# Kernel tuning notes

Measured on AMD Instinct MI355X. Metric: run time of the kernel, lower is better.

The kernel has to match this reference:

```python
import jax, jax.numpy as jnp
import numpy as np

KH = KW = 3
STRIDE = 1
PAD = 1
DIL = 1


def _bilinear_sample(x, py, px):
    """Zero-padded bilinear sampling.
    x: [B, C, H, W]; py, px: [B, K2, Ho, Wo] float sample coords.
    returns [B, C, K2, Ho, Wo].
    """
    B, C, H, W = x.shape
    y0 = jnp.floor(py)
    x0 = jnp.floor(px)
    wy1 = py - y0
    wx1 = px - x0
    wy0 = 1.0 - wy1
    wx0 = 1.0 - wx1
    xf = x.reshape(B, C, H * W)

    def gather(iy, ix):
        valid = (iy >= 0) & (iy <= H - 1) & (ix >= 0) & (ix <= W - 1)
        iyc = jnp.clip(iy, 0, H - 1).astype(jnp.int32)
        ixc = jnp.clip(ix, 0, W - 1).astype(jnp.int32)
        idx = (iyc * W + ixc).reshape(B, 1, -1)  # [B,1,K2*Ho*Wo]
        v = jnp.take_along_axis(xf, idx, axis=2)
        v = v.reshape(B, C, *iy.shape[1:])
        return v * valid[:, None].astype(x.dtype)

    return (gather(y0, x0) * (wy0 * wx0)[:, None]
            + gather(y0, x0 + 1) * (wy0 * wx1)[:, None]
            + gather(y0 + 1, x0) * (wy1 * wx0)[:, None]
            + gather(y0 + 1, x0 + 1) * (wy1 * wx1)[:, None])


def setup_inputs() -> dict:
    key = jax.random.key(0)
    k1, k2, k3, k4 = jax.random.split(key, 4)
    B, C, H, W = 8, 64, 128, 128
    Cout = 64
    K2 = KH * KW
    x = jax.random.normal(k1, (B, C, H, W), dtype=jnp.float32)
    offset = jax.random.normal(k2, (B, 2 * K2, H, W), dtype=jnp.float32)
    mask = jax.random.uniform(k3, (B, K2, H, W), dtype=jnp.float32)
    n = C * KH * KW
    stdv = 1.0 / np.sqrt(n)
    weight = jax.random.uniform(k4, (Cout, C, KH, KW), dtype=jnp.float32,
                                minval=-stdv, maxval=stdv)
    bias = jnp.zeros((Cout,), dtype=jnp.float32)
    return {"x": x, "offset": offset, "mask": mask, "weight": weight, "bias": bias}


def reference(x, offset, mask, weight, bias):
    B, C, H, W = x.shape
    Cout, Cin, kh, kw = weight.shape
    K2 = kh * kw
    Ho = (H + 2 * PAD - (DIL * (kh - 1) + 1)) // STRIDE + 1
    Wo = (W + 2 * PAD - (DIL * (kw - 1) + 1)) // STRIDE + 1
    # offset channels come interleaved per kernel location: ::2 -> x, 1::2 -> y
    off = offset.reshape(B, K2, 2, Ho, Wo)
    dx = off[:, :, 0]  # [B,K2,Ho,Wo]
    dy = off[:, :, 1]
    base_y = (STRIDE * jnp.arange(Ho) - PAD).astype(x.dtype)  # [Ho]
    base_x = (STRIDE * jnp.arange(Wo) - PAD).astype(x.dtype)  # [Wo]
    ky = (DIL * jnp.arange(kh)).astype(x.dtype)
    kx = (DIL * jnp.arange(kw)).astype(x.dtype)
    koff_y = jnp.repeat(ky, kw)  # [K2]
    koff_x = jnp.tile(kx, kh)    # [K2]
    py = base_y[None, None, :, None] + koff_y[None, :, None, None] + dy
    px = base_x[None, None, None, :] + koff_x[None, :, None, None] + dx
    sampled = _bilinear_sample(x, py, px)          # [B,C,K2,Ho,Wo]
    sampled = sampled * mask[:, None]              # modulation
    w = weight.reshape(Cout, Cin * K2)
    cols = sampled.reshape(B, Cin * K2, Ho, Wo)
    out = jnp.einsum('bqhw,oq->bohw', cols, w) + bias[None, :, None, None]
    return out
```

## Files before the change

kernel.cpp:

```cpp
#include <hip/hip_runtime.h>
#include <hip/hip_bf16.h>


constexpr int B    = 8;
constexpr int C    = 64;
constexpr int H    = 128;
constexpr int W    = 128;
constexpr int COUT = 64;
constexpr int K2   = 9;
constexpr int HW   = H * W;

typedef __attribute__((ext_vector_type(8))) short bf16x8;
typedef __attribute__((ext_vector_type(4))) float f32x4;

constexpr int LDSS = 72;

__global__ __launch_bounds__(256) void transpose_x_kernel(
    const float* __restrict__ x, short* __restrict__ xt) {
    __shared__ float tbuf[64][65];
    const int blk  = blockIdx.x;
    const int b    = blk >> 8;
    const int hwb  = (blk & 255) * 64;
    const int lane = threadIdx.x & 63;
    const int grp  = threadIdx.x >> 6;
    const float* xb = x + (size_t)b * C * HW;
#pragma unroll
    for (int r = 0; r < 16; ++r) {
        const int c = grp * 16 + r;
        tbuf[c][lane] = xb[c * HW + hwb + lane];
    }
    __syncthreads();
    short* xo = xt + (size_t)b * HW * C;
#pragma unroll
    for (int r = 0; r < 16; ++r) {
        const int hw_l = grp * 16 + r;
        union { __hip_bfloat16 h; short s; } u;
        u.h = __float2bfloat16(tbuf[lane][hw_l]);
        xo[(size_t)(hwb + hw_l) * C + lane] = u.s;
    }
}

__global__ __launch_bounds__(256) void pack_w_kernel(
    const float* __restrict__ w, short* __restrict__ wfrag) {
    int id = blockIdx.x * blockDim.x + threadIdx.x;
    if (id >= COUT * C * K2) return;
    const int j    = id & 7;
    const int lane = (id >> 3) & 63;
    const int mt   = (id >> 9) & 3;
    const int kk   = (id >> 11) & 1;
    const int k    = id >> 12;
    const int m    = mt * 16 + (lane & 15);
    const int q    = lane >> 4;
    const int c    = kk * 32 + q * 8 + j;
    union { __hip_bfloat16 h; short s; } u;
    u.h = __float2bfloat16(w[(m * C + c) * K2 + k]);
    wfrag[id] = u.s;
}

__global__ __launch_bounds__(256, 6) void mdcn_mfma_kernel(
    const short* __restrict__ xt,
    const float* __restrict__ offset,
    const float* __restrict__ mask,
    const short* __restrict__ wfrag,
    const float* __restrict__ bias,
    float* __restrict__ out) {

    __shared__ short smem[64 * LDSS];
    __shared__ float offs[2 * K2 * 64];
    __shared__ float msks[K2 * 64];

    const int wg   = blockIdx.x;
    const int b    = wg & 7;
    const int t    = wg >> 3;
    const int ho   = t >> 1;
    const int px0  = (t & 1) * 64;

    const int tid  = threadIdx.x;
    const int wave = tid >> 6;
    const int lane = tid & 63;
    const int col  = lane & 15;
    const int q    = lane >> 4;
    const int spx  = tid >> 2;
    const int cq   = (tid & 3) * 16;

    for (int f = tid; f < 2 * K2 * 64; f += 256) {
        const int ch = f >> 6, i = f & 63;
        offs[f] = offset[(((size_t)b * 2 * K2 + ch) * H + ho) * W + px0 + i];
    }
    for (int f = tid; f < K2 * 64; f += 256) {
        const int ch = f >> 6, i = f & 63;
        msks[f] = mask[(((size_t)b * K2 + ch) * H + ho) * W + px0 + i];
    }

    const short* xb = xt + (size_t)b * HW * C;
    f32x4 acc[4];
#pragma unroll
    for (int mt = 0; mt < 4; ++mt) acc[mt] = (f32x4)0.0f;

    __syncthreads();

    for (int k = 0; k < K2; ++k) {
        const int ky = k / 3, kx = k % 3;
        const float dx = offs[(2 * k    ) * 64 + spx];
        const float dy = offs[(2 * k + 1) * 64 + spx];
        const float mm = msks[k * 64 + spx];
        const int wo = px0 + spx;

        const float py = (float)(ho - 1 + ky) + dy;
        const float px = (float)(wo - 1 + kx) + dx;
        const float y0f = floorf(py), x0f = floorf(px);
        const float wy1 = py - y0f,   wx1 = px - x0f;
        const float wy0 = 1.0f - wy1, wx0 = 1.0f - wx1;
        const int iy0 = (int)y0f, ix0 = (int)x0f;
        const int iy1 = iy0 + 1,  ix1 = ix0 + 1;
        const bool vy0 = (iy0 >= 0) & (iy0 < H);
        const bool vy1 = (iy1 >= 0) & (iy1 < H);
        const bool vx0 = (ix0 >= 0) & (ix0 < W);
        const bool vx1 = (ix1 >= 0) & (ix1 < W);
        const float w00 = (vy0 & vx0) ? wy0 * wx0 * mm : 0.0f;
        const float w01 = (vy0 & vx1) ? wy0 * wx1 * mm : 0.0f;
        const float w10 = (vy1 & vx0) ? wy1 * wx0 * mm : 0.0f;
        const float w11 = (vy1 & vx1) ? wy1 * wx1 * mm : 0.0f;
        const int cy0 = min(max(iy0, 0), H - 1);
        const int cy1 = min(max(iy1, 0), H - 1);
        const int cx0 = min(max(ix0, 0), W - 1);
        const int cx1 = min(max(ix1, 0), W - 1);

        const short* s00 = xb + (cy0 * W + cx0) * C + cq;
        const short* s01 = xb + (cy0 * W + cx1) * C + cq;
        const short* s10 = xb + (cy1 * W + cx0) * C + cq;
        const short* s11 = xb + (cy1 * W + cx1) * C + cq;

        bf16x8 g00[2], g01[2], g10[2], g11[2];
#pragma unroll
        for (int j = 0; j < 2; ++j) {
            g00[j] = *(const bf16x8*)(s00 + j * 8);
            g01[j] = *(const bf16x8*)(s01 + j * 8);
            g10[j] = *(const bf16x8*)(s10 + j * 8);
            g11[j] = *(const bf16x8*)(s11 + j * 8);
        }

        short* sdst = smem + spx * LDSS + cq;
#pragma unroll
        for (int j = 0; j < 2; ++j) {
            union U8 { bf16x8 s; __hip_bfloat162 h2[4]; };
            U8 u00{g00[j]}, u01{g01[j]}, u10{g10[j]}, u11{g11[j]}, r;
#pragma unroll
            for (int p = 0; p < 4; ++p) {
                const float2 f00 = __bfloat1622float2(u00.h2[p]);
                const float2 f01 = __bfloat1622float2(u01.h2[p]);
                const float2 f10 = __bfloat1622float2(u10.h2[p]);
                const float2 f11 = __bfloat1622float2(u11.h2[p]);
                float2 v;
                v.x = w00 * f00.x + w01 * f01.x + w10 * f10.x + w11 * f11.x;
                v.y = w00 * f00.y + w01 * f01.y + w10 * f10.y + w11 * f11.y;
                r.h2[p] = __float22bfloat162_rn(v);
            }
            *(bf16x8*)(sdst + j * 8) = r.s;
        }
        __syncthreads();

        const bf16x8* wf = (const bf16x8*)wfrag;
#pragma unroll
        for (int kk = 0; kk < 2; ++kk) {
            const bf16x8 bfrag =
                *(const bf16x8*)(smem + (wave * 16 + col) * LDSS + kk * 32 + q * 8);
#pragma unroll
            for (int mt = 0; mt < 4; ++mt) {
                const bf16x8 afrag = wf[((k * 2 + kk) * 4 + mt) * 64 + lane];
                acc[mt] = __builtin_amdgcn_mfma_f32_16x16x32_bf16(
                    afrag, bfrag, acc[mt], 0, 0, 0);
            }
        }
        __syncthreads();
    }

    const int wo = px0 + wave * 16 + col;
#pragma unroll
    for (int mt = 0; mt < 4; ++mt) {
#pragma unroll
        for (int r = 0; r < 4; ++r) {
            const int o = mt * 16 + q * 4 + r;
            out[(((size_t)b * COUT + o) * H + ho) * W + wo] = acc[mt][r] + bias[o];
        }
    }
}

__global__ __launch_bounds__(256) void mdcn_direct_kernel(
    const float* __restrict__ x, const float* __restrict__ offset,
    const float* __restrict__ mask, const float* __restrict__ wsrc,
    const float* __restrict__ bias, float* __restrict__ out) {
    const int p  = blockIdx.x * blockDim.x + threadIdx.x;
    const int wo = p & (W - 1);
    const int ho = (p >> 7) & (H - 1);
    const int b  = p >> 14;
    float acc[COUT];
#pragma unroll
    for (int o = 0; o < COUT; ++o) acc[o] = bias[o];
    const float* xb = x + b * C * HW;
    for (int k = 0; k < K2; ++k) {
        const int ky = k / 3, kx = k % 3;
        const float dx = offset[((b * 2 * K2 + 2 * k    ) * H + ho) * W + wo];
        const float dy = offset[((b * 2 * K2 + 2 * k + 1) * H + ho) * W + wo];
        const float m  = mask  [((b * K2     + k        ) * H + ho) * W + wo];
        const float py = (float)(ho - 1 + ky) + dy;
        const float px = (float)(wo - 1 + kx) + dx;
        const float y0f = floorf(py), x0f = floorf(px);
        const float wy1 = py - y0f, wx1 = px - x0f;
        const float wy0 = 1.0f - wy1, wx0 = 1.0f - wx1;
        const int iy0 = (int)y0f, ix0 = (int)x0f;
        const int iy1 = iy0 + 1, ix1 = ix0 + 1;
        const bool vy0 = (iy0 >= 0) & (iy0 < H);
        const bool vy1 = (iy1 >= 0) & (iy1 < H);
        const bool vx0 = (ix0 >= 0) & (ix0 < W);
        const bool vx1 = (ix1 >= 0) & (ix1 < W);
        const float w00 = (vy0 & vx0) ? wy0 * wx0 * m : 0.0f;
        const float w01 = (vy0 & vx1) ? wy0 * wx1 * m : 0.0f;
        const float w10 = (vy1 & vx0) ? wy1 * wx0 * m : 0.0f;
        const float w11 = (vy1 & vx1) ? wy1 * wx1 * m : 0.0f;
        const int cy0 = min(max(iy0, 0), H - 1);
        const int cy1 = min(max(iy1, 0), H - 1);
        const int cx0 = min(max(ix0, 0), W - 1);
        const int cx1 = min(max(ix1, 0), W - 1);
        const int o00 = cy0 * W + cx0, o01 = cy0 * W + cx1;
        const int o10 = cy1 * W + cx0, o11 = cy1 * W + cx1;
        for (int c = 0; c < C; ++c) {
            const float* xp = xb + c * HW;
            const float val = w00 * xp[o00] + w01 * xp[o01] +
                              w10 * xp[o10] + w11 * xp[o11];
#pragma unroll
            for (int o = 0; o < COUT; ++o)
                acc[o] += wsrc[(o * C + c) * K2 + k] * val;
        }
    }
    float* op = out + ((size_t)b * COUT) * HW + ho * W + wo;
#pragma unroll
    for (int o = 0; o < COUT; ++o) op[o * HW] = acc[o];
}

extern "C" void kernel_launch(void* const* d_in, const int* in_sizes, int n_in,
                              void* d_out, int out_size, void* d_ws, size_t ws_size,
                              hipStream_t stream) {
    const float* x      = (const float*)d_in[0];
    const float* offset = (const float*)d_in[1];
    const float* mask   = (const float*)d_in[2];
    const float* weight = (const float*)d_in[3];
    const float* bias   = (const float*)d_in[4];
    float* out          = (float*)d_out;

    const size_t xt_bytes = (size_t)B * HW * C * sizeof(short);
    const size_t wf_bytes = (size_t)COUT * C * K2 * sizeof(short);
    if (ws_size >= xt_bytes + wf_bytes) {
        short* xt    = (short*)d_ws;
        short* wfrag = (short*)((char*)d_ws + xt_bytes);
        transpose_x_kernel<<<B * (HW / 64), 256, 0, stream>>>(x, xt);
        pack_w_kernel<<<(COUT * C * K2 + 255) / 256, 256, 0, stream>>>(weight, wfrag);
        mdcn_mfma_kernel<<<2 * B * H, 256, 0, stream>>>(xt, offset, mask, wfrag, bias, out);
    } else {
        mdcn_direct_kernel<<<(B * HW) / 256, 256, 0, stream>>>(
            x, offset, mask, weight, bias, out);
    }
}
```

Measured before the change: 152.7 us.

## Build MFMA B-fragments directly in registers, dropping LDS staging and barriers

Each lane now computes the bilinear samples for exactly the pixel/channel slice its MFMA B-fragment needs, so the LDS tile and both per-tap __syncthreads are removed. Offsets and mask are loaded straight from global memory into per-lane register arrays instead of being staged in shared memory. Launch bounds occupancy hint drops from 6 to 4 to allow more registers. The cost is redundant offset/weight computation across the 4 q-lanes sharing a pixel and higher register pressure.

```diff
diff --git a/kernel.cpp b/kernel.cpp
--- a/kernel.cpp
+++ b/kernel.cpp
@@ -12,8 +12,6 @@
 
 typedef __attribute__((ext_vector_type(8))) short bf16x8;
 typedef __attribute__((ext_vector_type(4))) float f32x4;
-
-constexpr int LDSS = 72;
 
 __global__ __launch_bounds__(256) void transpose_x_kernel(
     const float* __restrict__ x, short* __restrict__ xt) {
@@ -57,7 +55,7 @@
     wfrag[id] = u.s;
 }
 
-__global__ __launch_bounds__(256, 6) void mdcn_mfma_kernel(
+__global__ __launch_bounds__(256, 4) void mdcn_mfma_kernel(
     const short* __restrict__ xt,
     const float* __restrict__ offset,
     const float* __restrict__ mask,
@@ -65,10 +63,6 @@
     const float* __restrict__ bias,
     float* __restrict__ out) {
 
-    __shared__ short smem[64 * LDSS];
-    __shared__ float offs[2 * K2 * 64];
-    __shared__ float msks[K2 * 64];
-
     const int wg   = blockIdx.x;
     const int b    = wg & 7;
     const int t    = wg >> 3;
@@ -80,34 +74,28 @@
     const int lane = tid & 63;
     const int col  = lane & 15;
     const int q    = lane >> 4;
-    const int spx  = tid >> 2;
-    const int cq   = (tid & 3) * 16;
-
-    for (int f = tid; f < 2 * K2 * 64; f += 256) {
-        const int ch = f >> 6, i = f & 63;
-        offs[f] = offset[(((size_t)b * 2 * K2 + ch) * H + ho) * W + px0 + i];
-    }
-    for (int f = tid; f < K2 * 64; f += 256) {
-        const int ch = f >> 6, i = f & 63;
-        msks[f] = mask[(((size_t)b * K2 + ch) * H + ho) * W + px0 + i];
-    }
-
-    const short* xb = xt + (size_t)b * HW * C;
+    const int wo   = px0 + wave * 16 + col;
+
+    float dxs[K2], dys[K2], ms[K2];
+#pragma unroll
+    for (int k = 0; k < K2; ++k) {
+        dxs[k] = offset[(((size_t)b * 2 * K2 + 2 * k    ) * H + ho) * W + wo];
+        dys[k] = offset[(((size_t)b * 2 * K2 + 2 * k + 1) * H + ho) * W + wo];
+        ms[k]  = mask  [(((size_t)b * K2     + k        ) * H + ho) * W + wo];
+    }
+
+    const short*  xb = xt + (size_t)b * HW * C;
+    const bf16x8* wf = (const bf16x8*)wfrag;
+
     f32x4 acc[4];
 #pragma unroll
     for (int mt = 0; mt < 4; ++mt) acc[mt] = (f32x4)0.0f;
-
-    __syncthreads();
 
     for (int k = 0; k < K2; ++k) {
         const int ky = k / 3, kx = k % 3;
-        const float dx = offs[(2 * k    ) * 64 + spx];
-        const float dy = offs[(2 * k + 1) * 64 + spx];
-        const float mm = msks[k * 64 + spx];
-        const int wo = px0 + spx;
-
-        const float py = (float)(ho - 1 + ky) + dy;
-        const float px = (float)(wo - 1 + kx) + dx;
+        const float mm = ms[k];
+        const float py = (float)(ho - 1 + ky) + dys[k];
+        const float px = (float)(wo - 1 + kx) + dxs[k];
         const float y0f = floorf(py), x0f = floorf(px);
         const float wy1 = py - y0f,   wx1 = px - x0f;
         const float wy0 = 1.0f - wy1, wx0 = 1.0f - wx1;
@@ -125,26 +113,21 @@
         const int cy1 = min(max(iy1, 0), H - 1);
         const int cx0 = min(max(ix0, 0), W - 1);
         const int cx1 = min(max(ix1, 0), W - 1);
-
-        const short* s00 = xb + (cy0 * W + cx0) * C + cq;
-        const short* s01 = xb + (cy0 * W + cx1) * C + cq;
-        const short* s10 = xb + (cy1 * W + cx0) * C + cq;
-        const short* s11 = xb + (cy1 * W + cx1) * C + cq;
-
-        bf16x8 g00[2], g01[2], g10[2], g11[2];
-#pragma unroll
-        for (int j = 0; j < 2; ++j) {
-            g00[j] = *(const bf16x8*)(s00 + j * 8);
-            g01[j] = *(const bf16x8*)(s01 + j * 8);
-            g10[j] = *(const bf16x8*)(s10 + j * 8);
-            g11[j] = *(const bf16x8*)(s11 + j * 8);
-        }
-
-        short* sdst = smem + spx * LDSS + cq;
-#pragma unroll
-        for (int j = 0; j < 2; ++j) {
+        const int b00 = (cy0 * W + cx0) * C;
+        const int b01 = (cy0 * W + cx1) * C;
+        const int b10 = (cy1 * W + cx0) * C;
+        const int b11 = (cy1 * W + cx1) * C;
+
+        bf16x8 bfrag[2];
+#pragma unroll
+        for (int kk = 0; kk < 2; ++kk) {
+            const int co = kk * 32 + q * 8;
+            const bf16x8 g00 = *(const bf16x8*)(xb + b00 + co);
+            const bf16x8 g01 = *(const bf16x8*)(xb + b01 + co);
+            const bf16x8 g10 = *(const bf16x8*)(xb + b10 + co);
+            const bf16x8 g11 = *(const bf16x8*)(xb + b11 + co);
             union U8 { bf16x8 s; __hip_bfloat162 h2[4]; };
-            U8 u00{g00[j]}, u01{g01[j]}, u10{g10[j]}, u11{g11[j]}, r;
+            U8 u00{g00}, u01{g01}, u10{g10}, u11{g11}, rr;
 #pragma unroll
             for (int p = 0; p < 4; ++p) {
                 const float2 f00 = __bfloat1622float2(u00.h2[p]);
@@ -154,28 +137,20 @@
                 float2 v;
                 v.x = w00 * f00.x + w01 * f01.x + w10 * f10.x + w11 * f11.x;
                 v.y = w00 * f00.y + w01 * f01.y + w10 * f10.y + w11 * f11.y;
-                r.h2[p] = __float22bfloat162_rn(v);
+                rr.h2[p] = __float22bfloat162_rn(v);
             }
-            *(bf16x8*)(sdst + j * 8) = r.s;
+            bfrag[kk] = rr.s;
         }
-        __syncthreads();
-
-        const bf16x8* wf = (const bf16x8*)wfrag;
-#pragma unroll
-        for (int kk = 0; kk < 2; ++kk) {
-            const bf16x8 bfrag =
-                *(const bf16x8*)(smem + (wave * 16 + col) * LDSS + kk * 32 + q * 8);
-#pragma unroll
-            for (int mt = 0; mt < 4; ++mt) {
-                const bf16x8 afrag = wf[((k * 2 + kk) * 4 + mt) * 64 + lane];
+
+#pragma unroll
+        for (int kk = 0; kk < 2; ++kk)
+#pragma unroll
+            for (int mt = 0; mt < 4; ++mt)
                 acc[mt] = __builtin_amdgcn_mfma_f32_16x16x32_bf16(
-                    afrag, bfrag, acc[mt], 0, 0, 0);
-            }
-        }
-        __syncthreads();
-    }
-
-    const int wo = px0 + wave * 16 + col;
+                    wf[((k * 2 + kk) * 4 + mt) * 64 + lane], bfrag[kk],
+                    acc[mt], 0, 0, 0);
+    }
+
 #pragma unroll
     for (int mt = 0; mt < 4; ++mt) {
 #pragma unroll
```

Measured after the change: 184.1 us. 20.6% more time.

## Warp-specialize deformable conv into gather producers and MFMA consumers with double buffering

Applied to the files above, without the earlier changes.

The block grows to 512 threads. Four waves do the bilinear gather and write the interpolated bf16 columns into a double-buffered LDS tile. The other four waves load weight fragments and run the MFMA accumulation on the previous tile. The aim is to overlap the latency-heavy gather with the matrix multiply, where before each wave did both with two barriers per kernel tap. The cost is that only half the resident waves now issue gather loads, so memory-latency hiding for the gather may drop, and LDS use doubles.

```diff
diff --git a/kernel.cpp b/kernel.cpp
--- a/kernel.cpp
+++ b/kernel.cpp
@@ -57,7 +57,7 @@
     wfrag[id] = u.s;
 }
 
-__global__ __launch_bounds__(256, 6) void mdcn_mfma_kernel(
+__global__ __launch_bounds__(512, 4) void mdcn_pc_kernel(
     const short* __restrict__ xt,
     const float* __restrict__ offset,
     const float* __restrict__ mask,
@@ -65,7 +65,7 @@
     const float* __restrict__ bias,
     float* __restrict__ out) {
 
-    __shared__ short smem[64 * LDSS];
+    __shared__ short smem[2][64 * LDSS];
     __shared__ float offs[2 * K2 * 64];
     __shared__ float msks[K2 * 64];
 
@@ -77,111 +77,113 @@
 
     const int tid  = threadIdx.x;
     const int wave = tid >> 6;
-    const int lane = tid & 63;
-    const int col  = lane & 15;
-    const int q    = lane >> 4;
-    const int spx  = tid >> 2;
-    const int cq   = (tid & 3) * 16;
-
-    for (int f = tid; f < 2 * K2 * 64; f += 256) {
+
+    for (int f = tid; f < 2 * K2 * 64; f += 512) {
         const int ch = f >> 6, i = f & 63;
         offs[f] = offset[(((size_t)b * 2 * K2 + ch) * H + ho) * W + px0 + i];
     }
-    for (int f = tid; f < K2 * 64; f += 256) {
+    for (int f = tid; f < K2 * 64; f += 512) {
         const int ch = f >> 6, i = f & 63;
         msks[f] = mask[(((size_t)b * K2 + ch) * H + ho) * W + px0 + i];
     }
-
-    const short* xb = xt + (size_t)b * HW * C;
-    f32x4 acc[4];
-#pragma unroll
-    for (int mt = 0; mt < 4; ++mt) acc[mt] = (f32x4)0.0f;
-
     __syncthreads();
 
-    for (int k = 0; k < K2; ++k) {
-        const int ky = k / 3, kx = k % 3;
-        const float dx = offs[(2 * k    ) * 64 + spx];
-        const float dy = offs[(2 * k + 1) * 64 + spx];
-        const float mm = msks[k * 64 + spx];
-        const int wo = px0 + spx;
-
-        const float py = (float)(ho - 1 + ky) + dy;
-        const float px = (float)(wo - 1 + kx) + dx;
-        const float y0f = floorf(py), x0f = floorf(px);
-        const float wy1 = py - y0f,   wx1 = px - x0f;
-        const float wy0 = 1.0f - wy1, wx0 = 1.0f - wx1;
-        const int iy0 = (int)y0f, ix0 = (int)x0f;
-        const int iy1 = iy0 + 1,  ix1 = ix0 + 1;
-        const bool vy0 = (iy0 >= 0) & (iy0 < H);
-        const bool vy1 = (iy1 >= 0) & (iy1 < H);
-        const bool vx0 = (ix0 >= 0) & (ix0 < W);
-        const bool vx1 = (ix1 >= 0) & (ix1 < W);
-        const float w00 = (vy0 & vx0) ? wy0 * wx0 * mm : 0.0f;
-        const float w01 = (vy0 & vx1) ? wy0 * wx1 * mm : 0.0f;
-        const float w10 = (vy1 & vx0) ? wy1 * wx0 * mm : 0.0f;
-        const float w11 = (vy1 & vx1) ? wy1 * wx1 * mm : 0.0f;
-        const int cy0 = min(max(iy0, 0), H - 1);
-        const int cy1 = min(max(iy1, 0), H - 1);
-        const int cx0 = min(max(ix0, 0), W - 1);
-        const int cx1 = min(max(ix1, 0), W - 1);
-
-        const short* s00 = xb + (cy0 * W + cx0) * C + cq;
-        const short* s01 = xb + (cy0 * W + cx1) * C + cq;
-        const short* s10 = xb + (cy1 * W + cx0) * C + cq;
-        const short* s11 = xb + (cy1 * W + cx1) * C + cq;
-
-        bf16x8 g00[2], g01[2], g10[2], g11[2];
-#pragma unroll
-        for (int j = 0; j < 2; ++j) {
-            g00[j] = *(const bf16x8*)(s00 + j * 8);
-            g01[j] = *(const bf16x8*)(s01 + j * 8);
-            g10[j] = *(const bf16x8*)(s10 + j * 8);
-            g11[j] = *(const bf16x8*)(s11 + j * 8);
-        }
-
-        short* sdst = smem + spx * LDSS + cq;
-#pragma unroll
-        for (int j = 0; j < 2; ++j) {
-            union U8 { bf16x8 s; __hip_bfloat162 h2[4]; };
-            U8 u00{g00[j]}, u01{g01[j]}, u10{g10[j]}, u11{g11[j]}, r;
-#pragma unroll
-            for (int p = 0; p < 4; ++p) {
-                const float2 f00 = __bfloat1622float2(u00.h2[p]);
-                const float2 f01 = __bfloat1622float2(u01.h2[p]);
-                const float2 f10 = __bfloat1622float2(u10.h2[p]);
-                const float2 f11 = __bfloat1622float2(u11.h2[p]);
-                float2 v;
-                v.x = w00 * f00.x + w01 * f01.x + w10 * f10.x + w11 * f11.x;
-                v.y = w00 * f00.y + w01 * f01.y + w10 * f10.y + w11 * f11.y;
-                r.h2[p] = __float22bfloat162_rn(v);
+    if (wave < 4) {
+        const int spx = tid >> 2;
+        const int cq  = (tid & 3) * 16;
+        const int wo  = px0 + spx;
+        const short* xb = xt + (size_t)b * HW * C;
+
+        for (int k = 0; k < K2; ++k) {
+            const int ky = k / 3, kx = k % 3;
+            const float dx = offs[(2 * k    ) * 64 + spx];
+            const float dy = offs[(2 * k + 1) * 64 + spx];
+            const float mm = msks[k * 64 + spx];
+            const float py = (float)(ho - 1 + ky) + dy;
+            const float px = (float)(wo - 1 + kx) + dx;
+            const float y0f = floorf(py), x0f = floorf(px);
+            const float wy1 = py - y0f,   wx1 = px - x0f;
+            const float wy0 = 1.0f - wy1, wx0 = 1.0f - wx1;
+            const int iy0 = (int)y0f, ix0 = (int)x0f;
+            const int iy1 = iy0 + 1,  ix1 = ix0 + 1;
+            const bool vy0 = (iy0 >= 0) & (iy0 < H);
+            const bool vy1 = (iy1 >= 0) & (iy1 < H);
+            const bool vx0 = (ix0 >= 0) & (ix0 < W);
+            const bool vx1 = (ix1 >= 0) & (ix1 < W);
+            const float w00 = (vy0 & vx0) ? wy0 * wx0 * mm : 0.0f;
+            const float w01 = (vy0 & vx1) ? wy0 * wx1 * mm : 0.0f;
+            const float w10 = (vy1 & vx0) ? wy1 * wx0 * mm : 0.0f;
+            const float w11 = (vy1 & vx1) ? wy1 * wx1 * mm : 0.0f;
+            const int cy0 = min(max(iy0, 0), H - 1);
+            const int cy1 = min(max(iy1, 0), H - 1);
+            const int cx0 = min(max(ix0, 0), W - 1);
+            const int cx1 = min(max(ix1, 0), W - 1);
+            const short* s00 = xb + (cy0 * W + cx0) * C + cq;
+            const short* s01 = xb + (cy0 * W + cx1) * C + cq;
+            const short* s10 = xb + (cy1 * W + cx0) * C + cq;
+            const short* s11 = xb + (cy1 * W + cx1) * C + cq;
+
+            short* dst = &smem[k & 1][spx * LDSS + cq];
+#pragma unroll
+            for (int h = 0; h < 2; ++h) {
+                const bf16x8 g00 = *(const bf16x8*)(s00 + h * 8);
+                const bf16x8 g01 = *(const bf16x8*)(s01 + h * 8);
+                const bf16x8 g10 = *(const bf16x8*)(s10 + h * 8);
+                const bf16x8 g11 = *(const bf16x8*)(s11 + h * 8);
+                union U8 { bf16x8 s; __hip_bfloat162 h2[4]; };
+                U8 u00{g00}, u01{g01}, u10{g10}, u11{g11}, rr;
+#pragma unroll
+                for (int p = 0; p < 4; ++p) {
+                    const float2 f00 = __bfloat1622float2(u00.h2[p]);
+                    const float2 f01 = __bfloat1622float2(u01.h2[p]);
+                    const float2 f10 = __bfloat1622float2(u10.h2[p]);
+                    const float2 f11 = __bfloat1622float2(u11.h2[p]);
+                    float2 v;
+                    v.x = w00 * f00.x + w01 * f01.x + w10 * f10.x + w11 * f11.x;
+                    v.y = w00 * f00.y + w01 * f01.y + w10 * f10.y + w11 * f11.y;
+                    rr.h2[p] = __float22bfloat162_rn(v);
+                }
+                *(bf16x8*)(dst + h * 8) = rr.s;
             }
-            *(bf16x8*)(sdst + j * 8) = r.s;
-        }
-        __syncthreads();
-
+            __syncthreads();
+        }
+    } else {
+        const int widx = wave - 4;
+        const int lane = tid & 63;
+        const int col  = lane & 15;
+        const int q    = lane >> 4;
+        const int pix  = widx * 16 + col;
         const bf16x8* wf = (const bf16x8*)wfrag;
-#pragma unroll
-        for (int kk = 0; kk < 2; ++kk) {
-            const bf16x8 bfrag =
-                *(const bf16x8*)(smem + (wave * 16 + col) * LDSS + kk * 32 + q * 8);
-#pragma unroll
-            for (int mt = 0; mt < 4; ++mt) {
-                const bf16x8 afrag = wf[((k * 2 + kk) * 4 + mt) * 64 + lane];
-                acc[mt] = __builtin_amdgcn_mfma_f32_16x16x32_bf16(
-                    afrag, bfrag, acc[mt], 0, 0, 0);
+
+        f32x4 acc[4];
+#pragma unroll
+        for (int mt = 0; mt < 4; ++mt) acc[mt] = (f32x4)0.0f;
+
+        for (int k = 0; k < K2; ++k) {
+            __syncthreads();
+            bf16x8 af[8];
+#pragma unroll
+            for (int i = 0; i < 8; ++i) af[i] = wf[(k * 8 + i) * 64 + lane];
+#pragma unroll
+            for (int kk = 0; kk < 2; ++kk) {
+                const bf16x8 bfrag =
+                    *(const bf16x8*)(&smem[k & 1][pix * LDSS + kk * 32 + q * 8]);
+#pragma unroll
+                for (int mt = 0; mt < 4; ++mt)
+                    acc[mt] = __builtin_amdgcn_mfma_f32_16x16x32_bf16(
+                        af[kk * 4 + mt], bfrag, acc[mt], 0, 0, 0);
             }
         }
-        __syncthreads();
-    }
-
-    const int wo = px0 + wave * 16 + col;
-#pragma unroll
-    for (int mt = 0; mt < 4; ++mt) {
-#pragma unroll
-        for (int r = 0; r < 4; ++r) {
-            const int o = mt * 16 + q * 4 + r;
-            out[(((size_t)b * COUT + o) * H + ho) * W + wo] = acc[mt][r] + bias[o];
+
+        const int wo = px0 + pix;
+#pragma unroll
+        for (int mt = 0; mt < 4; ++mt) {
+#pragma unroll
+            for (int r = 0; r < 4; ++r) {
+                const int o = mt * 16 + q * 4 + r;
+                out[(((size_t)b * COUT + o) * H + ho) * W + wo] =
+                    acc[mt][r] + bias[o];
+            }
         }
     }
 }
@@ -255,7 +257,7 @@
         short* wfrag = (short*)((char*)d_ws + xt_bytes);
         transpose_x_kernel<<<B * (HW / 64), 256, 0, stream>>>(x, xt);
         pack_w_kernel<<<(COUT * C * K2 + 255) / 256, 256, 0, stream>>>(weight, wfrag);
-        mdcn_mfma_kernel<<<2 * B * H, 256, 0, stream>>>(xt, offset, mask, wfrag, bias, out);
+        mdcn_pc_kernel<<<2 * B * H, 512, 0, stream>>>(xt, offset, mask, wfrag, bias, out);
     } else {
         mdcn_direct_kernel<<<(B * HW) / 256, 256, 0, stream>>>(
             x, offset, mask, weight, bias, out);
```

After: 144.7 us. 1.06x faster.
